# Performance work log

Measured on AMD Instinct MI355X. Metric: run time of the kernel, lower is better.

## Reference

```python
import jax, jax.numpy as jnp
import numpy as np

N_NODES = 100000
N_EDGES = 1600000


def _gcn_layer(h, edge_row, edge_col, edge_val, W):
    # GraphConvolution (eval mode, dropout skipped):
    # support = h @ W ; out = spmm(adj, support)
    support = h @ W                                   # [N, d_out]
    msg = support[edge_col] * edge_val[:, None]       # [E, d_out] gather
    return jax.ops.segment_sum(msg, edge_row, num_segments=N_NODES)


def setup_inputs() -> dict:
    key = jax.random.key(0)
    ks = jax.random.split(key, 7)
    x = jax.random.normal(ks[0], (N_NODES, 256), dtype=jnp.float32)
    edge_row = jax.random.randint(ks[1], (N_EDGES,), 0, N_NODES, dtype=jnp.int32)
    edge_col = jax.random.randint(ks[2], (N_EDGES,), 0, N_NODES, dtype=jnp.int32)
    edge_val = jax.random.uniform(ks[3], (N_EDGES,), dtype=jnp.float32)
    W1 = jax.random.normal(ks[4], (256, 128), dtype=jnp.float32) * 0.05
    W2 = jax.random.normal(ks[5], (128, 64), dtype=jnp.float32) * 0.05
    W3 = jax.random.normal(ks[6], (128, 64), dtype=jnp.float32) * 0.05
    return {"x": x, "edge_row": edge_row, "edge_col": edge_col,
            "edge_val": edge_val, "W1": W1, "W2": W2, "W3": W3}


def reference(x, edge_row, edge_col, edge_val, W1, W2, W3):
    hidden1 = jax.nn.relu(_gcn_layer(x, edge_row, edge_col, edge_val, W1))
    mu = _gcn_layer(hidden1, edge_row, edge_col, edge_val, W2)      # act = identity
    logvar = _gcn_layer(hidden1, edge_row, edge_col, edge_val, W3)  # act = identity
    # reparameterize: z_mu = mean(mu); z_logvar = log(mean(exp(logvar)))
    z_mu = jnp.mean(mu)
    z_logvar = jnp.log(jnp.mean(jnp.exp(logvar)))
    return (z_mu, z_logvar)
```

## Files before the change

kernel.cpp:

```cpp
#include <hip/hip_runtime.h>
#include <cstdint>
#include <cstddef>

namespace {

constexpr int NN = 100000;
constexpr int NE = 1600000;
constexpr int DI = 256;
constexpr int DH = 128;
constexpr int DO = 64;
constexpr int EPB = 1024;
constexpr int NBA = (NE + EPB - 1) / EPB;
constexpr int NBUK = (NN + 255) / 256;
constexpr int EDOT_NB = NE / 256;
constexpr int SP3_NB = NN / 32;
constexpr int G1_NB = (NN + 127) / 128;
constexpr int PREP_NB = (DI * DH + DH * DO) / 256;

using bf16x8 = __attribute__((ext_vector_type(8))) short;
using f32x4  = __attribute__((ext_vector_type(4))) float;

__device__ inline unsigned short f2bf(float f) {
  unsigned int u = __float_as_uint(f);
  u += 0x7FFFu + ((u >> 16) & 1u);
  return (unsigned short)(u >> 16);
}
__device__ inline float bflo(unsigned int u) { return __uint_as_float(u << 16); }
__device__ inline float bfhi(unsigned int u) { return __uint_as_float(u & 0xffff0000u); }

__device__ inline void fma8(float* acc, const uint4 g, const float v) {
  acc[0] = fmaf(v, bflo(g.x), acc[0]); acc[1] = fmaf(v, bfhi(g.x), acc[1]);
  acc[2] = fmaf(v, bflo(g.y), acc[2]); acc[3] = fmaf(v, bfhi(g.y), acc[3]);
  acc[4] = fmaf(v, bflo(g.z), acc[4]); acc[5] = fmaf(v, bfhi(g.z), acc[5]);
  acc[6] = fmaf(v, bflo(g.w), acc[6]); acc[7] = fmaf(v, bfhi(g.w), acc[7]);
}

__device__ __forceinline__ void gl16(const void* g, void* l) {
  __builtin_amdgcn_global_load_lds(
      (const __attribute__((address_space(1))) void*)g,
      (__attribute__((address_space(3))) void*)l, 16, 0, 0);
}

__device__ __forceinline__ bf16x8 pack8(const f32x4 lo, const f32x4 hi) {
  bf16x8 r;
  r[0] = (short)f2bf(lo[0]); r[1] = (short)f2bf(lo[1]);
  r[2] = (short)f2bf(lo[2]); r[3] = (short)f2bf(lo[3]);
  r[4] = (short)f2bf(hi[0]); r[5] = (short)f2bf(hi[1]);
  r[6] = (short)f2bf(hi[2]); r[7] = (short)f2bf(hi[3]);
  return r;
}

template <int BM, int BN, int BK, bool ABF16>
__device__ __forceinline__ void gemm_block(const void* __restrict__ Ap,
                                           const unsigned short* __restrict__ Bt,
                                           unsigned short* __restrict__ C,
                                           int M, int K, int bx) {
  constexpr int ABYT = ABF16 ? 2 : 4;
  constexpr int SBA = BK * ABYT;
  constexpr int SBB = BK * 2;
  constexpr int ASZ = BM * SBA;
  constexpr int BSZ = BN * SBB;
  constexpr int STAGE = ASZ + BSZ;
  constexpr int OUTP = BN + 8;
  constexpr int EP = (BM * OUTP * 2 > STAGE) ? 2 : 1;
  constexpr int ROWS_P = BM / EP;
  constexpr int OUTB = ROWS_P * OUTP * 2;
  constexpr int LDSB = STAGE > OUTB ? STAGE : OUTB;
  constexpr int AMSK = (SBA / 16 - 1) > 7 ? 7 : (SBA / 16 - 1);
  constexpr int BMSK = (SBB / 16 - 1) > 7 ? 7 : (SBB / 16 - 1);
  __shared__ __align__(16) char lds[LDSB];
  char* const as_ = lds;
  char* const bs_ = lds + ASZ;

  const int tid = threadIdx.x;
  const int wid = tid >> 6;
  const int lane = tid & 63;
  const int l15 = lane & 15;
  const int lg = lane >> 4;
  const int amsk = (l15 & AMSK) << 4;
  const int bmsk = (l15 & BMSK) << 4;
  const int row0 = bx * BM;

  constexpr int NGA = ASZ / (256 * 16);
  constexpr int NGB = BSZ / (256 * 16);
  const char* Ab = (const char*)Ap;
  const char* Bb = (const char*)Bt;

  f32x4 acc[2][BN / 16];
#pragma unroll
  for (int a = 0; a < 2; ++a)
#pragma unroll
    for (int b = 0; b < BN / 16; ++b) acc[a][b] = (f32x4)0.f;

  const int nk = K / BK;
  for (int t = 0; t < nk; ++t) {
    const int k0 = t * BK;
#pragma unroll
    for (int j = 0; j < NGA; ++j) {
      const int d = (j * 256 + tid) * 16;
      const int row = d / SBA;
      const int u = (d % SBA) ^ ((row & AMSK) << 4);
      int grow = row0 + row;
      if (grow >= M) grow = M - 1;
      gl16(Ab + (size_t)grow * (size_t)(K * ABYT) + k0 * ABYT + u, as_ + d);
    }
#pragma unroll
    for (int j = 0; j < NGB; ++j) {
      const int d = (j * 256 + tid) * 16;
      const int n = d / SBB;
      const int u = (d % SBB) ^ ((n & BMSK) << 4);
      gl16(Bb + (size_t)n * (size_t)(K * 2) + k0 * 2 + u, bs_ + d);
    }
    __syncthreads();
#pragma unroll
    for (int kk = 0; kk < BK; kk += 32) {
      const int koff = kk + lg * 8;
      bf16x8 a0, a1;
      if constexpr (!ABF16) {
        const int b0 = (wid * 32 + l15) * SBA + koff * 4;
        const int b1 = b0 + 16 * SBA;
        const f32x4 q00 = *(const f32x4*)(as_ + (b0 ^ amsk));
        const f32x4 q01 = *(const f32x4*)(as_ + ((b0 ^ amsk) ^ 16));
        const f32x4 q10 = *(const f32x4*)(as_ + (b1 ^ amsk));
        const f32x4 q11 = *(const f32x4*)(as_ + ((b1 ^ amsk) ^ 16));
        a0 = pack8(q00, q01);
        a1 = pack8(q10, q11);
      } else {
        const int b0 = (wid * 32 + l15) * SBA + koff * 2;
        const int b1 = b0 + 16 * SBA;
        a0 = *(const bf16x8*)(as_ + (b0 ^ amsk));
        a1 = *(const bf16x8*)(as_ + (b1 ^ amsk));
      }
#pragma unroll
      for (int nf = 0; nf < BN / 16; ++nf) {
        const int n = nf * 16 + l15;
        const bf16x8 b = *(const bf16x8*)(bs_ + ((n * SBB + koff * 2) ^ bmsk));
        acc[0][nf] = __builtin_amdgcn_mfma_f32_16x16x32_bf16(a0, b, acc[0][nf], 0, 0, 0);
        acc[1][nf] = __builtin_amdgcn_mfma_f32_16x16x32_bf16(a1, b, acc[1][nf], 0, 0, 0);
      }
    }
    __syncthreads();
  }
  unsigned short* outl = (unsigned short*)lds;
#pragma unroll
  for (int pp = 0; pp < EP; ++pp) {
    if ((wid * 32) / ROWS_P == pp || EP == 1) {
#pragma unroll
      for (int mf = 0; mf < 2; ++mf)
#pragma unroll
        for (int nf = 0; nf < BN / 16; ++nf)
#pragma unroll
          for (int r = 0; r < 4; ++r) {
            const int row = wid * 32 + mf * 16 + lg * 4 + r;
            const int col = nf * 16 + l15;
            outl[(row - pp * ROWS_P) * OUTP + col] = f2bf(acc[mf][nf][r]);
          }
    }
    __syncthreads();
#pragma unroll
    for (int i = tid; i < ROWS_P * (BN / 8); i += 256) {
      const int m = i / (BN / 8), c8 = i % (BN / 8);
      const int row = row0 + pp * ROWS_P + m;
      if (row < M)
        *(float4*)(&C[(size_t)row * BN + c8 * 8]) = *(const float4*)(&outl[m * OUTP + c8 * 8]);
    }
    if (EP > 1) __syncthreads();
  }
}

__global__ __launch_bounds__(256) void k_prep(const float* __restrict__ W1,
                                              const float* __restrict__ W3,
                                              unsigned short* __restrict__ w1t,
                                              unsigned short* __restrict__ w3t) {
  const int i = blockIdx.x * 256 + threadIdx.x;
  if (i < DI * DH) {
    const int n = i / DI, k = i % DI;
    w1t[i] = f2bf(W1[k * DH + n]);
  } else {
    const int j = i - DI * DH;
    const int n = j / DH, k = j % DH;
    w3t[j] = f2bf(W3[k * DO + n]);
  }
}

__global__ __launch_bounds__(256) void k_passA(const int* __restrict__ erow,
                                               int* __restrict__ gcnt,
                                               unsigned short* __restrict__ rank8) {
  __shared__ int h[NBUK];
  const int tid = threadIdx.x, k = blockIdx.x;
  for (int i = tid; i < NBUK; i += 256) h[i] = 0;
  __syncthreads();
  const int e0 = k * EPB;
#pragma unroll
  for (int j = 0; j < 4; ++j) {
    const int e = e0 + j * 256 + tid;
    if (e < NE) rank8[e] = (unsigned short)atomicAdd(&h[erow[e] >> 8], 1);
  }
  __syncthreads();
  for (int i = tid; i < NBUK; i += 256) gcnt[(size_t)k * NBUK + i] = h[i];
}

__global__ __launch_bounds__(256) void k_passB1(const int* __restrict__ gcnt,
                                                int* __restrict__ boff,
                                                int* __restrict__ btot) {
  const int b = blockIdx.x, t = threadIdx.x;
  int v[7];
  int s = 0;
#pragma unroll
  for (int j = 0; j < 7; ++j) {
    const int k = t * 7 + j;
    v[j] = (k < NBA) ? gcnt[(size_t)k * NBUK + b] : 0;
    s += v[j];
  }
  __shared__ int ps[256];
  ps[t] = s;
  __syncthreads();
  for (int off = 1; off < 256; off <<= 1) {
    int x = (t >= off) ? ps[t - off] : 0;
    __syncthreads();
    ps[t] += x;
    __syncthreads();
  }
  int excl = ps[t] - s;
  if (t == 255) btot[b] = ps[255];
#pragma unroll
  for (int j = 0; j < 7; ++j) {
    const int k = t * 7 + j;
    if (k < NBA) boff[(size_t)b * NBA + k] = excl;
    excl += v[j];
  }
}

__global__ __launch_bounds__(256) void k_passB2(const int* __restrict__ btot,
                                                int* __restrict__ bbase,
                                                int* __restrict__ rowptr,
                                                const float* __restrict__ W2,
                                                float* __restrict__ w2s) {
  if (blockIdx.x == 1) {
    const int kk = threadIdx.x;
    if (kk < DH) {
      float s = 0.f;
      for (int d = 0; d < DO; ++d) s += W2[kk * DO + d];
      w2s[kk] = s;
    }
    return;
  }
  __shared__ int sdat[512];
  const int t = threadIdx.x;
  sdat[t] = (t < NBUK) ? btot[t] : 0;
  sdat[t + 256] = (t + 256 < NBUK) ? btot[t + 256] : 0;
  __syncthreads();
  for (int off = 1; off < 512; off <<= 1) {
    const int x0 = (t >= off) ? sdat[t - off] : 0;
    const int x1 = (t + 256 >= off) ? sdat[t + 256 - off] : 0;
    __syncthreads();
    sdat[t] += x0;
    sdat[t + 256] += x1;
    __syncthreads();
  }
  if (t == 0) { bbase[0] = 0; rowptr[NN] = NE; }
  bbase[t + 1] = sdat[t];
  if (t + 257 <= NBUK) bbase[t + 257] = sdat[t + 256];
}

__global__ __launch_bounds__(256) void k_cg1(const float* __restrict__ x,
                                             const unsigned short* __restrict__ w1t,
                                             unsigned short* __restrict__ sup,
                                             const int* __restrict__ erow,
                                             const int* __restrict__ ecol,
                                             const float* __restrict__ eval,
                                             const unsigned short* __restrict__ rank8,
                                             const int* __restrict__ boff,
                                             const int* __restrict__ bbase,
                                             uint2* __restrict__ scv) {
  const int b = blockIdx.x;
  if (b < G1_NB) {
    gemm_block<128, 128, 32, false>(x, w1t, sup, NN, DI, b);
  } else {
    const int k = b - G1_NB;
    const int e0 = k * EPB;
    const int tid = threadIdx.x;
#pragma unroll
    for (int j = 0; j < 4; ++j) {
      const int e = e0 + j * 256 + tid;
      if (e < NE) {
        const int r = erow[e];
        const int bu = r >> 8;
        const int pos = bbase[bu] + boff[(size_t)bu * NBA + k] + (int)rank8[e];
        scv[pos] = make_uint2(((unsigned)(r & 255) << 17) | (unsigned)ecol[e],
                              __float_as_uint(eval[e]));
      }
    }
  }
}

__global__ __launch_bounds__(256) void k_passD(const uint2* __restrict__ scv,
                                               const int* __restrict__ bbase,
                                               int* __restrict__ rowptr,
                                               int2* __restrict__ cpk) {
  const int b = blockIdx.x, t = threadIdx.x;
  const int lo = bbase[b], hi = bbase[b + 1];
  __shared__ int c1[256], sc[256];
  c1[t] = 0;
  __syncthreads();
  for (int e = lo + t; e < hi; e += 256) atomicAdd(&c1[scv[e].x >> 17], 1);
  __syncthreads();
  const int my = c1[t];
  sc[t] = my;
  __syncthreads();
  for (int off = 1; off < 256; off <<= 1) {
    const int xx = (t >= off) ? sc[t - off] : 0;
    __syncthreads();
    sc[t] += xx;
    __syncthreads();
  }
  const int ro = sc[t] - my;
  const int gr = b * 256 + t;
  if (gr < NN) rowptr[gr] = lo + ro;
  c1[t] = 0;
  sc[t] = ro;
  __syncthreads();
  for (int e = lo + t; e < hi; e += 256) {
    const uint2 q = scv[e];
    const int i = (int)(q.x >> 17);
    const int p = lo + sc[i] + atomicAdd(&c1[i], 1);
    cpk[p] = make_int2((int)(q.x & 0x1FFFFu), (int)q.y);
  }
}

__global__ __launch_bounds__(256) void k_spmm1(const unsigned short* __restrict__ sup1,
                                               const int* __restrict__ rowptr,
                                               const int2* __restrict__ cpk,
                                               const float* __restrict__ w2s,
                                               unsigned short* __restrict__ h1,
                                               float* __restrict__ hw) {
  const int tid = threadIdx.x;
  const int lane = tid & 15;
  const int r = blockIdx.x * 16 + (tid >> 4);
  const int e0 = rowptr[r];
  const int e1 = rowptr[r + 1];
  const uint4* s8 = reinterpret_cast<const uint4*>(sup1);
  float aA[8] = {0,0,0,0,0,0,0,0}, aB[8] = {0,0,0,0,0,0,0,0};
  float aC[8] = {0,0,0,0,0,0,0,0}, aD[8] = {0,0,0,0,0,0,0,0};
  int e = e0;
  for (; e + 4 <= e1; e += 4) {
    const int2 p0 = cpk[e],     p1 = cpk[e + 1];
    const int2 p2 = cpk[e + 2], p3 = cpk[e + 3];
    const uint4 g0 = s8[(size_t)p0.x * 16 + lane];
    const uint4 g1 = s8[(size_t)p1.x * 16 + lane];
    const uint4 g2 = s8[(size_t)p2.x * 16 + lane];
    const uint4 g3 = s8[(size_t)p3.x * 16 + lane];
    fma8(aA, g0, __int_as_float(p0.y));
    fma8(aB, g1, __int_as_float(p1.y));
    fma8(aC, g2, __int_as_float(p2.y));
    fma8(aD, g3, __int_as_float(p3.y));
  }
  if (e + 2 <= e1) {
    const int2 p0 = cpk[e], p1 = cpk[e + 1];
    const uint4 g0 = s8[(size_t)p0.x * 16 + lane];
    const uint4 g1 = s8[(size_t)p1.x * 16 + lane];
    fma8(aA, g0, __int_as_float(p0.y));
    fma8(aB, g1, __int_as_float(p1.y));
    e += 2;
  }
  if (e < e1) {
    const int2 p0 = cpk[e];
    const uint4 g0 = s8[(size_t)p0.x * 16 + lane];
    fma8(aC, g0, __int_as_float(p0.y));
  }
  float acc[8];
#pragma unroll
  for (int j = 0; j < 8; ++j) acc[j] = fmaxf((aA[j] + aB[j]) + (aC[j] + aD[j]), 0.f);
  uint4 o;
  o.x = (unsigned)f2bf(acc[0]) | ((unsigned)f2bf(acc[1]) << 16);
  o.y = (unsigned)f2bf(acc[2]) | ((unsigned)f2bf(acc[3]) << 16);
  o.z = (unsigned)f2bf(acc[4]) | ((unsigned)f2bf(acc[5]) << 16);
  o.w = (unsigned)f2bf(acc[6]) | ((unsigned)f2bf(acc[7]) << 16);
  reinterpret_cast<uint4*>(h1)[(size_t)r * 16 + lane] = o;
  const float4 wlo = reinterpret_cast<const float4*>(w2s)[lane * 2];
  const float4 whi = reinterpret_cast<const float4*>(w2s)[lane * 2 + 1];
  float p = acc[0] * wlo.x + acc[1] * wlo.y + acc[2] * wlo.z + acc[3] * wlo.w +
            acc[4] * whi.x + acc[5] * whi.y + acc[6] * whi.z + acc[7] * whi.w;
#pragma unroll
  for (int off = 8; off > 0; off >>= 1) p += __shfl_down(p, off, 16);
  if (lane == 0) hw[r] = p;
}

__global__ __launch_bounds__(256) void k_g2_edot(const unsigned short* __restrict__ h1,
                                                 const unsigned short* __restrict__ w3t,
                                                 unsigned short* __restrict__ sup,
                                                 const int* __restrict__ ecol,
                                                 const float* __restrict__ eval,
                                                 const float* __restrict__ hw,
                                                 float* __restrict__ pzmu) {
  const int b = blockIdx.x;
  if (b % 9 == 0) {
    gemm_block<128, 64, 64, true>(h1, w3t, sup, NN, DH, b / 9);
  } else {
    const int eb = (b / 9) * 8 + (b % 9) - 1;
    if (eb < EDOT_NB) {
      __shared__ float red[256];
      const int i = eb * 256 + threadIdx.x;
      red[threadIdx.x] = eval[i] * hw[ecol[i]];
      __syncthreads();
      for (int off = 128; off > 0; off >>= 1) {
        if (threadIdx.x < off) red[threadIdx.x] += red[threadIdx.x + off];
        __syncthreads();
      }
      if (threadIdx.x == 0) pzmu[eb] = red[0];
    }
  }
}

__global__ __launch_bounds__(256) void k_spmm3(const unsigned short* __restrict__ sup3,
                                               const int* __restrict__ rowptr,
                                               const int2* __restrict__ cpk,
                                               float* __restrict__ pexp) {
  const int tid = threadIdx.x;
  const int lane = tid & 7;
  const int r = blockIdx.x * 32 + (tid >> 3);
  const int e0 = rowptr[r];
  const int e1 = rowptr[r + 1];
  const uint4* s8 = reinterpret_cast<const uint4*>(sup3);
  float aA[8] = {0,0,0,0,0,0,0,0}, aB[8] = {0,0,0,0,0,0,0,0};
  float aC[8] = {0,0,0,0,0,0,0,0}, aD[8] = {0,0,0,0,0,0,0,0};
  int e = e0;
  for (; e + 4 <= e1; e += 4) {
    const int2 p0 = cpk[e],     p1 = cpk[e + 1];
    const int2 p2 = cpk[e + 2], p3 = cpk[e + 3];
    const uint4 g0 = s8[(size_t)p0.x * 8 + lane];
    const uint4 g1 = s8[(size_t)p1.x * 8 + lane];
    const uint4 g2 = s8[(size_t)p2.x * 8 + lane];
    const uint4 g3 = s8[(size_t)p3.x * 8 + lane];
    fma8(aA, g0, __int_as_float(p0.y));
    fma8(aB, g1, __int_as_float(p1.y));
    fma8(aC, g2, __int_as_float(p2.y));
    fma8(aD, g3, __int_as_float(p3.y));
  }
  if (e + 2 <= e1) {
    const int2 p0 = cpk[e], p1 = cpk[e + 1];
    const uint4 g0 = s8[(size_t)p0.x * 8 + lane];
    const uint4 g1 = s8[(size_t)p1.x * 8 + lane];
    fma8(aA, g0, __int_as_float(p0.y));
    fma8(aB, g1, __int_as_float(p1.y));
    e += 2;
  }
  if (e < e1) {
    const int2 p0 = cpk[e];
    const uint4 g0 = s8[(size_t)p0.x * 8 + lane];
    fma8(aC, g0, __int_as_float(p0.y));
  }
  float p = 0.f;
#pragma unroll
  for (int j = 0; j < 8; ++j) p += expf((aA[j] + aB[j]) + (aC[j] + aD[j]));
#pragma unroll
  for (int off = 4; off > 0; off >>= 1) p += __shfl_down(p, off, 8);
  __shared__ float part[32];
  if (lane == 0) part[tid >> 3] = p;
  __syncthreads();
  if (tid == 0) {
    float s = 0.f;
#pragma unroll
    for (int i = 0; i < 32; ++i) s += part[i];
    pexp[blockIdx.x] = s;
  }
}

__global__ __launch_bounds__(256) void k_final(const float* __restrict__ pzmu, int nz,
                                               const float* __restrict__ pexp, int ne,
                                               float* __restrict__ out) {
  __shared__ float red[256];
  const int t = threadIdx.x;
  float s1 = 0.f, s2 = 0.f;
  for (int i = t; i < nz; i += 256) s1 += pzmu[i];
  for (int i = t; i < ne; i += 256) s2 += pexp[i];
  red[t] = s1;
  __syncthreads();
  for (int off = 128; off > 0; off >>= 1) {
    if (t < off) red[t] += red[t + off];
    __syncthreads();
  }
  const float tot1 = red[0];
  __syncthreads();
  red[t] = s2;
  __syncthreads();
  for (int off = 128; off > 0; off >>= 1) {
    if (t < off) red[t] += red[t + off];
    __syncthreads();
  }
  if (t == 0) {
    const float denom = (float)NN * (float)DO;
    out[0] = tot1 / denom;
    out[1] = logf(red[0] / denom);
  }
}

}

extern "C" void kernel_launch(void* const* d_in, const int* in_sizes, int n_in,
                              void* d_out, int out_size, void* d_ws, size_t ws_size,
                              hipStream_t stream) {
  const float* x    = (const float*)d_in[0];
  const int*   erow = (const int*)d_in[1];
  const int*   ecol = (const int*)d_in[2];
  const float* eval = (const float*)d_in[3];
  const float* W1   = (const float*)d_in[4];
  const float* W2   = (const float*)d_in[5];
  const float* W3   = (const float*)d_in[6];
  float* out = (float*)d_out;

  char* p = (char*)d_ws;
  auto alloc = [&](size_t bytes) -> void* {
    void* r = (void*)p;
    p += (bytes + 255) & ~(size_t)255;
    return r;
  };
  unsigned short* sup = (unsigned short*)alloc((size_t)NN * DH * 2);
  unsigned short* h1  = (unsigned short*)alloc((size_t)NN * DH * 2);
  int2*  cpk    = (int2*)alloc((size_t)NE * 8);
  uint2* scv    = (uint2*)alloc((size_t)NE * 8);
  unsigned short* rank8 = (unsigned short*)alloc((size_t)NE * 2);
  int*   rowptr = (int*)alloc((size_t)(NN + 1) * 4);
  int*   gcnt   = (int*)alloc((size_t)NBA * NBUK * 4);
  int*   boff   = (int*)alloc((size_t)NBUK * NBA * 4);
  int*   btot   = (int*)alloc((size_t)NBUK * 4);
  int*   bbase  = (int*)alloc((size_t)(NBUK + 1) * 4);
  float* hw     = (float*)alloc((size_t)NN * 4);
  float* w2s    = (float*)alloc(DH * 4);
  unsigned short* w1t = (unsigned short*)alloc((size_t)DH * DI * 2);
  unsigned short* w3t = (unsigned short*)alloc((size_t)DO * DH * 2);
  float* pexp   = (float*)alloc(SP3_NB * 4);
  float* pzmu   = (float*)alloc(EDOT_NB * 4);

  k_prep<<<PREP_NB, 256, 0, stream>>>(W1, W3, w1t, w3t);

  k_passA<<<NBA, 256, 0, stream>>>(erow, gcnt, rank8);
  k_passB1<<<NBUK, 256, 0, stream>>>(gcnt, boff, btot);
  k_passB2<<<2, 256, 0, stream>>>(btot, bbase, rowptr, W2, w2s);
  k_cg1<<<G1_NB + NBA, 256, 0, stream>>>(x, w1t, sup, erow, ecol, eval,
                                         rank8, boff, bbase, scv);
  k_passD<<<NBUK, 256, 0, stream>>>(scv, bbase, rowptr, cpk);

  k_spmm1<<<NN / 16, 256, 0, stream>>>(sup, rowptr, cpk, w2s, h1, hw);

  k_g2_edot<<<G1_NB * 9, 256, 0, stream>>>(h1, w3t, sup, ecol, eval, hw, pzmu);

  k_spmm3<<<NN / 32, 256, 0, stream>>>(sup, rowptr, cpk, pexp);

  k_final<<<1, 256, 0, stream>>>(pzmu, EDOT_NB, pexp, SP3_NB, out);
}
```

Baseline: 200.3 us.

## Replace LDS-staged GEMM tiles with per-wave register strip GEMM

Both fused GEMMs now have each wave compute a 32-row strip by loading A and B fragments straight from global memory into registers, with no LDS staging, barriers or swizzle. Output is written directly as scattered 2-byte stores instead of coalesced 16-byte stores through LDS. This removes the synchronisation and LDS traffic, but B fragments are re-read from global or L2 by every wave and the stores are less coalesced. Block counts stay the same because each block still covers 128 rows.

```diff
diff --git a/kernel.cpp b/kernel.cpp
--- a/kernel.cpp
+++ b/kernel.cpp
@@ -14,7 +14,8 @@
 constexpr int NBUK = (NN + 255) / 256;
 constexpr int EDOT_NB = NE / 256;
 constexpr int SP3_NB = NN / 32;
-constexpr int G1_NB = (NN + 127) / 128;
+constexpr int NSTRIP = NN / 32;
+constexpr int G1_NB = (NSTRIP + 3) / 4;
 constexpr int PREP_NB = (DI * DH + DH * DO) / 256;
 
 using bf16x8 = __attribute__((ext_vector_type(8))) short;
@@ -33,12 +34,6 @@
   acc[2] = fmaf(v, bflo(g.y), acc[2]); acc[3] = fmaf(v, bfhi(g.y), acc[3]);
   acc[4] = fmaf(v, bflo(g.z), acc[4]); acc[5] = fmaf(v, bfhi(g.z), acc[5]);
   acc[6] = fmaf(v, bflo(g.w), acc[6]); acc[7] = fmaf(v, bfhi(g.w), acc[7]);
-}
-
-__device__ __forceinline__ void gl16(const void* g, void* l) {
-  __builtin_amdgcn_global_load_lds(
-      (const __attribute__((address_space(1))) void*)g,
-      (__attribute__((address_space(3))) void*)l, 16, 0, 0);
 }
 
 __device__ __forceinline__ bf16x8 pack8(const f32x4 lo, const f32x4 hi) {
@@ -50,122 +45,59 @@
   return r;
 }
 
-template <int BM, int BN, int BK, bool ABF16>
-__device__ __forceinline__ void gemm_block(const void* __restrict__ Ap,
+template <int KD, int ND, bool ABF16>
+__device__ __forceinline__ void gemm_strip(const void* __restrict__ Ap,
                                            const unsigned short* __restrict__ Bt,
                                            unsigned short* __restrict__ C,
-                                           int M, int K, int bx) {
-  constexpr int ABYT = ABF16 ? 2 : 4;
-  constexpr int SBA = BK * ABYT;
-  constexpr int SBB = BK * 2;
-  constexpr int ASZ = BM * SBA;
-  constexpr int BSZ = BN * SBB;
-  constexpr int STAGE = ASZ + BSZ;
-  constexpr int OUTP = BN + 8;
-  constexpr int EP = (BM * OUTP * 2 > STAGE) ? 2 : 1;
-  constexpr int ROWS_P = BM / EP;
-  constexpr int OUTB = ROWS_P * OUTP * 2;
-  constexpr int LDSB = STAGE > OUTB ? STAGE : OUTB;
-  constexpr int AMSK = (SBA / 16 - 1) > 7 ? 7 : (SBA / 16 - 1);
-  constexpr int BMSK = (SBB / 16 - 1) > 7 ? 7 : (SBB / 16 - 1);
-  __shared__ __align__(16) char lds[LDSB];
-  char* const as_ = lds;
-  char* const bs_ = lds + ASZ;
-
-  const int tid = threadIdx.x;
-  const int wid = tid >> 6;
-  const int lane = tid & 63;
+                                           int s) {
+  constexpr int NF = ND / 16;
+  const int lane = threadIdx.x & 63;
   const int l15 = lane & 15;
   const int lg = lane >> 4;
-  const int amsk = (l15 & AMSK) << 4;
-  const int bmsk = (l15 & BMSK) << 4;
-  const int row0 = bx * BM;
-
-  constexpr int NGA = ASZ / (256 * 16);
-  constexpr int NGB = BSZ / (256 * 16);
-  const char* Ab = (const char*)Ap;
-  const char* Bb = (const char*)Bt;
-
-  f32x4 acc[2][BN / 16];
+  const int r0 = s * 32;
+  const int koff0 = lg * 8;
+
+  f32x4 acc[2][NF];
 #pragma unroll
   for (int a = 0; a < 2; ++a)
 #pragma unroll
-    for (int b = 0; b < BN / 16; ++b) acc[a][b] = (f32x4)0.f;
-
-  const int nk = K / BK;
-  for (int t = 0; t < nk; ++t) {
-    const int k0 = t * BK;
-#pragma unroll
-    for (int j = 0; j < NGA; ++j) {
-      const int d = (j * 256 + tid) * 16;
-      const int row = d / SBA;
-      const int u = (d % SBA) ^ ((row & AMSK) << 4);
-      int grow = row0 + row;
-      if (grow >= M) grow = M - 1;
-      gl16(Ab + (size_t)grow * (size_t)(K * ABYT) + k0 * ABYT + u, as_ + d);
+    for (int b = 0; b < NF; ++b) acc[a][b] = (f32x4)0.f;
+
+#pragma unroll 2
+  for (int k0 = 0; k0 < KD; k0 += 32) {
+    const int koff = k0 + koff0;
+    bf16x8 a0, a1;
+    if constexpr (!ABF16) {
+      const float* A = (const float*)Ap;
+      const float* p0 = &A[(size_t)(r0 + l15) * KD + koff];
+      const float* p1 = &A[(size_t)(r0 + l15 + 16) * KD + koff];
+      const f32x4 q00 = *(const f32x4*)(p0);
+      const f32x4 q01 = *(const f32x4*)(p0 + 4);
+      const f32x4 q10 = *(const f32x4*)(p1);
+      const f32x4 q11 = *(const f32x4*)(p1 + 4);
+      a0 = pack8(q00, q01);
+      a1 = pack8(q10, q11);
+    } else {
+      const unsigned short* A = (const unsigned short*)Ap;
+      a0 = *(const bf16x8*)(&A[(size_t)(r0 + l15) * KD + koff]);
+      a1 = *(const bf16x8*)(&A[(size_t)(r0 + l15 + 16) * KD + koff]);
     }
 #pragma unroll
-    for (int j = 0; j < NGB; ++j) {
-      const int d = (j * 256 + tid) * 16;
-      const int n = d / SBB;
-      const int u = (d % SBB) ^ ((n & BMSK) << 4);
-      gl16(Bb + (size_t)n * (size_t)(K * 2) + k0 * 2 + u, bs_ + d);
+    for (int nf = 0; nf < NF; ++nf) {
+      const bf16x8 b = *(const bf16x8*)(&Bt[(size_t)(nf * 16 + l15) * KD + koff]);
+      acc[0][nf] = __builtin_amdgcn_mfma_f32_16x16x32_bf16(a0, b, acc[0][nf], 0, 0, 0);
+      acc[1][nf] = __builtin_amdgcn_mfma_f32_16x16x32_bf16(a1, b, acc[1][nf], 0, 0, 0);
     }
-    __syncthreads();
-#pragma unroll
-    for (int kk = 0; kk < BK; kk += 32) {
-      const int koff = kk + lg * 8;
-      bf16x8 a0, a1;
-      if constexpr (!ABF16) {
-        const int b0 = (wid * 32 + l15) * SBA + koff * 4;
-        const int b1 = b0 + 16 * SBA;
-        const f32x4 q00 = *(const f32x4*)(as_ + (b0 ^ amsk));
-        const f32x4 q01 = *(const f32x4*)(as_ + ((b0 ^ amsk) ^ 16));
-        const f32x4 q10 = *(const f32x4*)(as_ + (b1 ^ amsk));
-        const f32x4 q11 = *(const f32x4*)(as_ + ((b1 ^ amsk) ^ 16));
-        a0 = pack8(q00, q01);
-        a1 = pack8(q10, q11);
-      } else {
-        const int b0 = (wid * 32 + l15) * SBA + koff * 2;
-        const int b1 = b0 + 16 * SBA;
-        a0 = *(const bf16x8*)(as_ + (b0 ^ amsk));
-        a1 = *(const bf16x8*)(as_ + (b1 ^ amsk));
+  }
+#pragma unroll
+  for (int mf = 0; mf < 2; ++mf)
+#pragma unroll
+    for (int nf = 0; nf < NF; ++nf)
+#pragma unroll
+      for (int rr = 0; rr < 4; ++rr) {
+        const int row = r0 + mf * 16 + lg * 4 + rr;
+        C[(size_t)row * ND + nf * 16 + l15] = f2bf(acc[mf][nf][rr]);
       }
-#pragma unroll
-      for (int nf = 0; nf < BN / 16; ++nf) {
-        const int n = nf * 16 + l15;
-        const bf16x8 b = *(const bf16x8*)(bs_ + ((n * SBB + koff * 2) ^ bmsk));
-        acc[0][nf] = __builtin_amdgcn_mfma_f32_16x16x32_bf16(a0, b, acc[0][nf], 0, 0, 0);
-        acc[1][nf] = __builtin_amdgcn_mfma_f32_16x16x32_bf16(a1, b, acc[1][nf], 0, 0, 0);
-      }
-    }
-    __syncthreads();
-  }
-  unsigned short* outl = (unsigned short*)lds;
-#pragma unroll
-  for (int pp = 0; pp < EP; ++pp) {
-    if ((wid * 32) / ROWS_P == pp || EP == 1) {
-#pragma unroll
-      for (int mf = 0; mf < 2; ++mf)
-#pragma unroll
-        for (int nf = 0; nf < BN / 16; ++nf)
-#pragma unroll
-          for (int r = 0; r < 4; ++r) {
-            const int row = wid * 32 + mf * 16 + lg * 4 + r;
-            const int col = nf * 16 + l15;
-            outl[(row - pp * ROWS_P) * OUTP + col] = f2bf(acc[mf][nf][r]);
-          }
-    }
-    __syncthreads();
-#pragma unroll
-    for (int i = tid; i < ROWS_P * (BN / 8); i += 256) {
-      const int m = i / (BN / 8), c8 = i % (BN / 8);
-      const int row = row0 + pp * ROWS_P + m;
-      if (row < M)
-        *(float4*)(&C[(size_t)row * BN + c8 * 8]) = *(const float4*)(&outl[m * OUTP + c8 * 8]);
-    }
-    if (EP > 1) __syncthreads();
-  }
 }
 
 __global__ __launch_bounds__(256) void k_prep(const float* __restrict__ W1,
@@ -275,7 +207,8 @@
                                              uint2* __restrict__ scv) {
   const int b = blockIdx.x;
   if (b < G1_NB) {
-    gemm_block<128, 128, 32, false>(x, w1t, sup, NN, DI, b);
+    const int s = b * 4 + (threadIdx.x >> 6);
+    if (s < NSTRIP) gemm_strip<DI, DH, false>(x, w1t, sup, s);
   } else {
     const int k = b - G1_NB;
     const int e0 = k * EPB;
@@ -395,7 +328,8 @@
                                                  float* __restrict__ pzmu) {
   const int b = blockIdx.x;
   if (b % 9 == 0) {
-    gemm_block<128, 64, 64, true>(h1, w3t, sup, NN, DH, b / 9);
+    const int s = (b / 9) * 4 + (threadIdx.x >> 6);
+    if (s < NSTRIP) gemm_strip<DH, DO, true>(h1, w3t, sup, s);
   } else {
     const int eb = (b / 9) * 8 + (b % 9) - 1;
     if (eb < EDOT_NB) {
```

After: 223.3 us. 11.5% more time.
